# Performance work log

Measured on AMD Instinct MI355X. Metric: run time of the kernel, lower is better.

The kernel has to match this reference:

```python
import jax, jax.numpy as jnp
import numpy as np

SEQ = 110          # input_size1 = sample_width*2
HALF = SEQ // 2    # 55
N_EMBD = 102       # n_chrom + 2
HEAD = 192

def _cross_half_mask():
    # attention allowed only between the two halves (same-half blocks masked)
    idx = jnp.arange(SEQ)
    same_half = (idx[:, None] < HALF) == (idx[None, :] < HALF)
    return same_half  # True where attention is DISALLOWED

def setup_inputs() -> dict:
    key = jax.random.key(0)
    k1, k2, k3, k4 = jax.random.split(key, 4)
    B = 8192
    x = jax.random.normal(k1, (B, SEQ, N_EMBD), dtype=jnp.float32)
    Wq = jax.random.normal(k2, (N_EMBD, HEAD), dtype=jnp.float32) * (N_EMBD ** -0.5)
    Wk = jax.random.normal(k3, (N_EMBD, HEAD), dtype=jnp.float32) * (N_EMBD ** -0.5)
    Wv = jax.random.normal(k4, (N_EMBD, HEAD), dtype=jnp.float32) * (N_EMBD ** -0.5)
    return {"x": x, "Wq": Wq, "Wk": Wk, "Wv": Wv}

def reference(x, Wq, Wk, Wv):
    # q,k,v: [B, S, H]
    q = x @ Wq
    k = x @ Wk
    v = x @ Wv
    scale = HEAD ** -0.5
    scores = jnp.einsum('bsh,bth->bst', q, k) * scale  # [B, S, S]
    mask = _cross_half_mask()                           # [S, S] True = masked
    scores = jnp.where(mask, -jnp.inf, scores)
    attn = jax.nn.softmax(scores, axis=-1)
    # dropout is identity at inference (p=0.15 at train)
    out = jnp.einsum('bst,bth->bsh', attn, v)           # [B, S, H]
    return out
```

## Files before the change

### kernel.cpp

```cpp
#include <hip/hip_runtime.h>
#include <hip/hip_bf16.h>

#define SEQ   110
#define HALFS 55
#define EMB   102
#define HEAD  192

typedef short bf16x8 __attribute__((ext_vector_type(8)));
typedef float f32x4  __attribute__((ext_vector_type(4)));

#define XS    104
#define XTILE (64 * XS)
#define PS    72
#define MTS   128
#define MTROWS 112
#define MT_SHORTS (MTROWS * MTS)
#define WES   128

__device__ __forceinline__ short f2bf(float f) {
    unsigned u = __float_as_uint(f);
    unsigned r = u + 0x7fffu + ((u >> 16) & 1u);
    return (short)(r >> 16);
}
__device__ __forceinline__ unsigned pk2(float a, float b) {
    return ((unsigned)(unsigned short)f2bf(b) << 16) | (unsigned short)f2bf(a);
}

__global__ void prep(const float* __restrict__ Wq, const float* __restrict__ Wk,
                     const float* __restrict__ Wv, short* __restrict__ ws) {
    int flat = blockIdx.x * 256 + threadIdx.x;
    if (flat < MT_SHORTS) {
        int i = flat >> 7, j = flat & 127;
        float v = 0.0f;
        if (i < EMB && j < EMB) {
            const float4* q4 = (const float4*)(Wq + j * HEAD);
            const float4* k4 = (const float4*)(Wk + i * HEAD);
            float s = 0.0f;
            #pragma unroll 4
            for (int h4 = 0; h4 < HEAD / 4; ++h4) {
                float4 a = q4[h4], b = k4[h4];
                s += a.x * b.x + a.y * b.y + a.z * b.z + a.w * b.w;
            }
            v = s * 0.07216878364870322f;
        }
        ws[flat] = f2bf(v);
    } else if (flat < MT_SHORTS + HEAD * WES) {
        int idx = flat - MT_SHORTS;
        int h = idx >> 7, e = idx & 127;
        float v = (e < EMB) ? Wv[e * HEAD + h] : 0.0f;
        ws[flat] = f2bf(v);
    }
}

__global__ __launch_bounds__(512, 2)
void attn_head(const float* __restrict__ x, const short* __restrict__ ws,
               float* __restrict__ out, int B) {
    const int tid  = threadIdx.x;
    const int w8   = tid >> 6;
    const int h    = w8 >> 2;
    const int w4   = w8 & 3;
    const int lane = tid & 63;
    const int g    = lane >> 4;
    const int r    = lane & 15;

    __shared__ __attribute__((aligned(16))) short u[4 * XTILE];
    __shared__ __attribute__((aligned(16))) short P_lds[2][64 * PS];

    short* xh = u + h * XTILE;
    short* xo = u + (h ^ 1) * XTILE;
    short* yh = u + (2 + h) * XTILE;
    short* Ph = P_lds[h];

    const short* Mt  = ws;
    const short* WvT = ws + MT_SHORTS;

    bf16x8 wvf[3][4];
    #pragma unroll
    for (int mi = 0; mi < 3; ++mi) {
        const int hrow = 16 * (w4 + 4 * mi) + r;
        #pragma unroll
        for (int kk = 0; kk < 4; ++kk)
            wvf[mi][kk] = *(const bf16x8*)(WvT + hrow * WES + 32 * kk + 8 * g);
    }

    {
        unsigned long long* z = (unsigned long long*)u;
        if (tid < 468) z[(tid < 234 ? 1430 : 2860) + tid] = 0ull;
        if (tid < 110)
            *(unsigned*)(u + (tid & 1) * XTILE + (tid >> 1) * XS + 102) = 0u;
    }

    unsigned xv0[6], xv1[6];
    auto loadx = [&](int batch) {
        const float4* xb4 = (const float4*)(x + (size_t)batch * (SEQ * EMB));
        #pragma unroll
        for (int it = 0; it < 6; ++it) {
            int i4 = tid + it * 512;
            if (i4 < 2805) { float4 v = xb4[i4]; xv0[it] = pk2(v.x, v.y); xv1[it] = pk2(v.z, v.w); }
        }
    };
    auto stagex = [&]() {
        #pragma unroll
        for (int it = 0; it < 6; ++it) {
            int i4 = tid + it * 512;
            if (i4 < 2805) {
                int fc  = i4 * 4;
                int row = (int)(((unsigned long long)fc * 41121ull) >> 22);
                int e   = fc - row * EMB;
                int tile = row >= HALFS;
                int lr   = row - HALFS * tile;
                int ba   = tile * XTILE + lr * XS + e;
                if (e == 100) {
                    int rowb  = row + 1;
                    int tileb = rowb >= HALFS;
                    int lrb   = rowb - HALFS * tileb;
                    *(unsigned*)(u + ba) = xv0[it];
                    *(unsigned*)(u + tileb * XTILE + lrb * XS) = xv1[it];
                } else {
                    uint2 t2; t2.x = xv0[it]; t2.y = xv1[it];
                    *(uint2*)(u + ba) = t2;
                }
            }
        }
    };

    loadx(blockIdx.x);
    const int stride = (int)gridDim.x;

    bf16x8 ax[4][4];
    bf16x8 zz = {};

    #pragma unroll 1
    for (int p = blockIdx.x; p < B; p += stride) {
        stagex();
        __syncthreads();

        bf16x8 am[2][4];
        #pragma unroll
        for (int mi2 = 0; mi2 < 2; ++mi2) {
            const int mt = w4 + 4 * mi2;
            #pragma unroll
            for (int kk = 0; kk < 4; ++kk)
                am[mi2][kk] = (mt < 7) ? *(const bf16x8*)(Mt + (16 * mt + r) * MTS + 32 * kk + 8 * g) : zz;
        }

        #pragma unroll
        for (int stl = 0; stl < 4; ++stl) {
            const short* xb = xh + (16 * stl + r) * XS;
            bf16x8 bx[4];
            #pragma unroll
            for (int kk = 0; kk < 3; ++kk) bx[kk] = *(const bf16x8*)(xb + 32 * kk + 8 * g);
            bx[3] = zz;
            if (g == 0) bx[3] = *(const bf16x8*)(xb + 96);
            #pragma unroll
            for (int mi2 = 0; mi2 < 2; ++mi2) {
                const int mt = w4 + 4 * mi2;
                if (mt < 7) {
                    f32x4 acc = {0.f, 0.f, 0.f, 0.f};
                    #pragma unroll
                    for (int kk = 0; kk < 4; ++kk)
                        acc = __builtin_amdgcn_mfma_f32_16x16x32_bf16(am[mi2][kk], bx[kk], acc, 0, 0, 0);
                    if (mt < 6 || g < 2) {
                        uint2 t2; t2.x = pk2(acc[0], acc[1]); t2.y = pk2(acc[2], acc[3]);
                        *(uint2*)(yh + (16 * stl + r) * XS + 16 * mt + 4 * g) = t2;
                    }
                }
            }
        }

        #pragma unroll
        for (int mt = 0; mt < 4; ++mt) {
            const short* xb = xo + (16 * mt + r) * XS;
            #pragma unroll
            for (int kk = 0; kk < 3; ++kk) ax[mt][kk] = *(const bf16x8*)(xb + 32 * kk + 8 * g);
            ax[mt][3] = zz;
            if (g == 0) ax[mt][3] = *(const bf16x8*)(xb + 96);
        }

        unsigned vpk[4][3][2];
        #pragma unroll
        for (int st = 0; st < 4; ++st) {
            #pragma unroll
            for (int mi = 0; mi < 3; ++mi) {
                f32x4 acc = {0.f, 0.f, 0.f, 0.f};
                #pragma unroll
                for (int kk = 0; kk < 4; ++kk)
                    acc = __builtin_amdgcn_mfma_f32_16x16x32_bf16(ax[st][kk], wvf[mi][kk], acc, 0, 0, 0);
                vpk[st][mi][0] = pk2(acc[0], acc[1]);
                vpk[st][mi][1] = pk2(acc[2], acc[3]);
            }
        }
        const int src0 = ((g & 1) << 5) + r;
        const int src1 = src0 + 16;
        const bool hi  = (g >> 1) != 0;
        bf16x8 va[3][2];
        #pragma unroll
        for (int mi = 0; mi < 3; ++mi) {
            unsigned e00 = (unsigned)__shfl((int)vpk[0][mi][0], src0), e01 = (unsigned)__shfl((int)vpk[0][mi][1], src0);
            unsigned e02 = (unsigned)__shfl((int)vpk[0][mi][0], src1), e03 = (unsigned)__shfl((int)vpk[0][mi][1], src1);
            unsigned f00 = (unsigned)__shfl((int)vpk[1][mi][0], src0), f01 = (unsigned)__shfl((int)vpk[1][mi][1], src0);
            unsigned f02 = (unsigned)__shfl((int)vpk[1][mi][0], src1), f03 = (unsigned)__shfl((int)vpk[1][mi][1], src1);
            uint4 u0;
            u0.x = hi ? f00 : e00; u0.y = hi ? f01 : e01; u0.z = hi ? f02 : e02; u0.w = hi ? f03 : e03;
            unsigned e10 = (unsigned)__shfl((int)vpk[2][mi][0], src0), e11 = (unsigned)__shfl((int)vpk[2][mi][1], src0);
            unsigned e12 = (unsigned)__shfl((int)vpk[2][mi][0], src1), e13 = (unsigned)__shfl((int)vpk[2][mi][1], src1);
            unsigned f10 = (unsigned)__shfl((int)vpk[3][mi][0], src0), f11 = (unsigned)__shfl((int)vpk[3][mi][1], src0);
            unsigned f12 = (unsigned)__shfl((int)vpk[3][mi][0], src1), f13 = (unsigned)__shfl((int)vpk[3][mi][1], src1);
            uint4 u1;
            u1.x = hi ? f10 : e10; u1.y = hi ? f11 : e11; u1.z = hi ? f12 : e12; u1.w = hi ? f13 : e13;
            __builtin_memcpy(&va[mi][0], &u0, 16);
            __builtin_memcpy(&va[mi][1], &u1, 16);
        }

        __syncthreads();

        if (p + stride < B) loadx(p + stride);

        {
            const short* yb = yh + (16 * w4 + r) * XS;
            bf16x8 by[4];
            #pragma unroll
            for (int kk = 0; kk < 3; ++kk) by[kk] = *(const bf16x8*)(yb + 32 * kk + 8 * g);
            by[3] = zz;
            if (g == 0) by[3] = *(const bf16x8*)(yb + 96);

            float sc[4][4];
            #pragma unroll
            for (int mt = 0; mt < 4; ++mt) {
                f32x4 acc = {0.f, 0.f, 0.f, 0.f};
                #pragma unroll
                for (int kk = 0; kk < 4; ++kk)
                    acc = __builtin_amdgcn_mfma_f32_16x16x32_bf16(ax[mt][kk], by[kk], acc, 0, 0, 0);
                #pragma unroll
                for (int j = 0; j < 4; ++j) sc[mt][j] = acc[j];
            }
            #pragma unroll
            for (int j = 0; j < 4; ++j)
                if (48 + 4 * g + j >= HALFS) sc[3][j] = -1e30f;

            float mx = -1e30f;
            #pragma unroll
            for (int mt = 0; mt < 4; ++mt) {
                #pragma unroll
                for (int j = 0; j < 4; ++j) mx = fmaxf(mx, sc[mt][j]);
            }
            mx = fmaxf(mx, __shfl_xor(mx, 16));
            mx = fmaxf(mx, __shfl_xor(mx, 32));
            float pr[4][4];
            float sum = 0.f;
            #pragma unroll
            for (int mt = 0; mt < 4; ++mt) {
                #pragma unroll
                for (int j = 0; j < 4; ++j) { pr[mt][j] = __expf(sc[mt][j] - mx); sum += pr[mt][j]; }
            }
            sum += __shfl_xor(sum, 16);
            sum += __shfl_xor(sum, 32);
            float rs = 1.0f / sum;

            #pragma unroll
            for (int mt = 0; mt < 4; ++mt) {
                uint2 t2;
                t2.x = pk2(pr[mt][0] * rs, pr[mt][1] * rs);
                t2.y = pk2(pr[mt][2] * rs, pr[mt][3] * rs);
                *(uint2*)(Ph + (16 * w4 + r) * PS + 16 * mt + 4 * g) = t2;
            }
        }
        __syncthreads();

        const size_t obase = (size_t)p * (SEQ * HEAD) + (size_t)(h * HALFS) * HEAD;
        #pragma unroll
        for (int c = 0; c < 4; ++c) {
            const short* pb = Ph + (16 * c + r) * PS + 8 * g;
            bf16x8 bp0 = *(const bf16x8*)(pb);
            bf16x8 bp1 = *(const bf16x8*)(pb + 32);
            const int srow  = 16 * c + r;
            const bool valid = srow < HALFS;
            float* orow = out + obase + (size_t)srow * HEAD;
            #pragma unroll
            for (int mi = 0; mi < 3; ++mi) {
                f32x4 acc = {0.f, 0.f, 0.f, 0.f};
                acc = __builtin_amdgcn_mfma_f32_16x16x32_bf16(va[mi][0], bp0, acc, 0, 0, 0);
                acc = __builtin_amdgcn_mfma_f32_16x16x32_bf16(va[mi][1], bp1, acc, 0, 0, 0);
                if (valid) {
                    float4 st4; st4.x = acc[0]; st4.y = acc[1]; st4.z = acc[2]; st4.w = acc[3];
                    *(float4*)(orow + 16 * (w4 + 4 * mi) + 4 * g) = st4;
                }
            }
        }
        __syncthreads();
    }
}

extern "C" void kernel_launch(void* const* d_in, const int* in_sizes, int n_in,
                              void* d_out, int out_size, void* d_ws, size_t ws_size,
                              hipStream_t stream) {
    const float* x  = (const float*)d_in[0];
    const float* Wq = (const float*)d_in[1];
    const float* Wk = (const float*)d_in[2];
    const float* Wv = (const float*)d_in[3];
    short* ws = (short*)d_ws;
    int B = in_sizes[0] / (SEQ * EMB);
    int prep_elems = MT_SHORTS + HEAD * WES;
    prep<<<(prep_elems + 255) / 256, 256, 0, stream>>>(Wq, Wk, Wv, ws);
    attn_head<<<512, 512, 0, stream>>>(x, ws, (float*)d_out, B);
}
```

Measured before the change: 303.1 us.

## Keep projected Y in registers, restructure loop to cut LDS and barriers

Each wave now computes its own 16-row slice of the x·M projection directly, using Mt fragments loaded in the inner loop. The result is redistributed through lane shuffles into B-operand fragments instead of being written to an LDS Y tile and read back. This removes half of the x LDS buffer and two of the four barriers per iteration. The global prefetch of the next sample is issued at the start of the iteration and staged into LDS after the barrier, overlapping with the P·V output phase. The cost is more global/L2 reads of Mt per iteration, higher register pressure, and a tighter correctness dependency on barrier placement for the staged x buffer.

```diff
diff --git a/kernel.cpp b/kernel.cpp
--- a/kernel.cpp
+++ b/kernel.cpp
@@ -63,12 +63,11 @@
     const int g    = lane >> 4;
     const int r    = lane & 15;
 
-    __shared__ __attribute__((aligned(16))) short u[4 * XTILE];
+    __shared__ __attribute__((aligned(16))) short u[2 * XTILE];
     __shared__ __attribute__((aligned(16))) short P_lds[2][64 * PS];
 
     short* xh = u + h * XTILE;
     short* xo = u + (h ^ 1) * XTILE;
-    short* yh = u + (2 + h) * XTILE;
     short* Ph = P_lds[h];
 
     const short* Mt  = ws;
@@ -125,47 +124,58 @@
     };
 
     loadx(blockIdx.x);
+    stagex();
     const int stride = (int)gridDim.x;
 
     bf16x8 ax[4][4];
     bf16x8 zz = {};
+    const int src0 = ((g & 1) << 5) + r;
+    const int src1 = src0 + 16;
+    const bool hi  = (g >> 1) != 0;
 
     #pragma unroll 1
     for (int p = blockIdx.x; p < B; p += stride) {
-        stagex();
         __syncthreads();
 
-        bf16x8 am[2][4];
-        #pragma unroll
-        for (int mi2 = 0; mi2 < 2; ++mi2) {
-            const int mt = w4 + 4 * mi2;
-            #pragma unroll
-            for (int kk = 0; kk < 4; ++kk)
-                am[mi2][kk] = (mt < 7) ? *(const bf16x8*)(Mt + (16 * mt + r) * MTS + 32 * kk + 8 * g) : zz;
-        }
-
-        #pragma unroll
-        for (int stl = 0; stl < 4; ++stl) {
-            const short* xb = xh + (16 * stl + r) * XS;
-            bf16x8 bx[4];
+        if (p + stride < B) loadx(p + stride);
+
+        bf16x8 bx[4];
+        {
+            const short* xb = xh + (16 * w4 + r) * XS;
             #pragma unroll
             for (int kk = 0; kk < 3; ++kk) bx[kk] = *(const bf16x8*)(xb + 32 * kk + 8 * g);
             bx[3] = zz;
             if (g == 0) bx[3] = *(const bf16x8*)(xb + 96);
-            #pragma unroll
-            for (int mi2 = 0; mi2 < 2; ++mi2) {
-                const int mt = w4 + 4 * mi2;
-                if (mt < 7) {
-                    f32x4 acc = {0.f, 0.f, 0.f, 0.f};
-                    #pragma unroll
-                    for (int kk = 0; kk < 4; ++kk)
-                        acc = __builtin_amdgcn_mfma_f32_16x16x32_bf16(am[mi2][kk], bx[kk], acc, 0, 0, 0);
-                    if (mt < 6 || g < 2) {
-                        uint2 t2; t2.x = pk2(acc[0], acc[1]); t2.y = pk2(acc[2], acc[3]);
-                        *(uint2*)(yh + (16 * stl + r) * XS + 16 * mt + 4 * g) = t2;
-                    }
-                }
-            }
+        }
+
+        unsigned vyp[8][2];
+        #pragma unroll
+        for (int mt = 0; mt < 7; ++mt) {
+            f32x4 acc = {0.f, 0.f, 0.f, 0.f};
+            #pragma unroll
+            for (int kk = 0; kk < 4; ++kk) {
+                bf16x8 am = *(const bf16x8*)(Mt + (16 * mt + r) * MTS + 32 * kk + 8 * g);
+                acc = __builtin_amdgcn_mfma_f32_16x16x32_bf16(am, bx[kk], acc, 0, 0, 0);
+            }
+            vyp[mt][0] = pk2(acc[0], acc[1]);
+            vyp[mt][1] = pk2(acc[2], acc[3]);
+        }
+        vyp[7][0] = 0u; vyp[7][1] = 0u;
+
+        bf16x8 by[4];
+        #pragma unroll
+        for (int kk = 0; kk < 4; ++kk) {
+            unsigned e0 = (unsigned)__shfl((int)vyp[2 * kk][0],     src0);
+            unsigned e1 = (unsigned)__shfl((int)vyp[2 * kk][1],     src0);
+            unsigned e2 = (unsigned)__shfl((int)vyp[2 * kk][0],     src1);
+            unsigned e3 = (unsigned)__shfl((int)vyp[2 * kk][1],     src1);
+            unsigned f0 = (unsigned)__shfl((int)vyp[2 * kk + 1][0], src0);
+            unsigned f1 = (unsigned)__shfl((int)vyp[2 * kk + 1][1], src0);
+            unsigned f2 = (unsigned)__shfl((int)vyp[2 * kk + 1][0], src1);
+            unsigned f3 = (unsigned)__shfl((int)vyp[2 * kk + 1][1], src1);
+            uint4 q;
+            q.x = hi ? f0 : e0; q.y = hi ? f1 : e1; q.z = hi ? f2 : e2; q.w = hi ? f3 : e3;
+            __builtin_memcpy(&by[kk], &q, 16);
         }
 
         #pragma unroll
@@ -175,6 +185,49 @@
             for (int kk = 0; kk < 3; ++kk) ax[mt][kk] = *(const bf16x8*)(xb + 32 * kk + 8 * g);
             ax[mt][3] = zz;
             if (g == 0) ax[mt][3] = *(const bf16x8*)(xb + 96);
+        }
+
+        {
+            float sc[4][4];
+            #pragma unroll
+            for (int mt = 0; mt < 4; ++mt) {
+                f32x4 acc = {0.f, 0.f, 0.f, 0.f};
+                #pragma unroll
+                for (int kk = 0; kk < 4; ++kk)
+                    acc = __builtin_amdgcn_mfma_f32_16x16x32_bf16(ax[mt][kk], by[kk], acc, 0, 0, 0);
+                #pragma unroll
+                for (int j = 0; j < 4; ++j) sc[mt][j] = acc[j];
+            }
+            #pragma unroll
+            for (int j = 0; j < 4; ++j)
+                if (48 + 4 * g + j >= HALFS) sc[3][j] = -1e30f;
+
+            float mx = -1e30f;
+            #pragma unroll
+            for (int mt = 0; mt < 4; ++mt) {
+                #pragma unroll
+                for (int j = 0; j < 4; ++j) mx = fmaxf(mx, sc[mt][j]);
+            }
+            mx = fmaxf(mx, __shfl_xor(mx, 16));
+            mx = fmaxf(mx, __shfl_xor(mx, 32));
+            float pr[4][4];
+            float sum = 0.f;
+            #pragma unroll
+            for (int mt = 0; mt < 4; ++mt) {
+                #pragma unroll
+                for (int j = 0; j < 4; ++j) { pr[mt][j] = __expf(sc[mt][j] - mx); sum += pr[mt][j]; }
+            }
+            sum += __shfl_xor(sum, 16);
+            sum += __shfl_xor(sum, 32);
+            float rs = 1.0f / sum;
+
+            #pragma unroll
+            for (int mt = 0; mt < 4; ++mt) {
+                uint2 t2;
+                t2.x = pk2(pr[mt][0] * rs, pr[mt][1] * rs);
+                t2.y = pk2(pr[mt][2] * rs, pr[mt][3] * rs);
+                *(uint2*)(Ph + (16 * w4 + r) * PS + 16 * mt + 4 * g) = t2;
+            }
         }
 
         unsigned vpk[4][3][2];
@@ -190,9 +243,6 @@
                 vpk[st][mi][1] = pk2(acc[2], acc[3]);
             }
         }
-        const int src0 = ((g & 1) << 5) + r;
-        const int src1 = src0 + 16;
-        const bool hi  = (g >> 1) != 0;
         bf16x8 va[3][2];
         #pragma unroll
         for (int mi = 0; mi < 3; ++mi) {
@@ -214,58 +264,7 @@
 
         __syncthreads();
 
-        if (p + stride < B) loadx(p + stride);
-
-        {
-            const short* yb = yh + (16 * w4 + r) * XS;
-            bf16x8 by[4];
-            #pragma unroll
-            for (int kk = 0; kk < 3; ++kk) by[kk] = *(const bf16x8*)(yb + 32 * kk + 8 * g);
-            by[3] = zz;
-            if (g == 0) by[3] = *(const bf16x8*)(yb + 96);
-
-            float sc[4][4];
-            #pragma unroll
-            for (int mt = 0; mt < 4; ++mt) {
-                f32x4 acc = {0.f, 0.f, 0.f, 0.f};
-                #pragma unroll
-                for (int kk = 0; kk < 4; ++kk)
-                    acc = __builtin_amdgcn_mfma_f32_16x16x32_bf16(ax[mt][kk], by[kk], acc, 0, 0, 0);
-                #pragma unroll
-                for (int j = 0; j < 4; ++j) sc[mt][j] = acc[j];
-            }
-            #pragma unroll
-            for (int j = 0; j < 4; ++j)
-                if (48 + 4 * g + j >= HALFS) sc[3][j] = -1e30f;
-
-            float mx = -1e30f;
-            #pragma unroll
-            for (int mt = 0; mt < 4; ++mt) {
-                #pragma unroll
-                for (int j = 0; j < 4; ++j) mx = fmaxf(mx, sc[mt][j]);
-            }
-            mx = fmaxf(mx, __shfl_xor(mx, 16));
-            mx = fmaxf(mx, __shfl_xor(mx, 32));
-            float pr[4][4];
-            float sum = 0.f;
-            #pragma unroll
-            for (int mt = 0; mt < 4; ++mt) {
-                #pragma unroll
-                for (int j = 0; j < 4; ++j) { pr[mt][j] = __expf(sc[mt][j] - mx); sum += pr[mt][j]; }
-            }
-            sum += __shfl_xor(sum, 16);
-            sum += __shfl_xor(sum, 32);
-            float rs = 1.0f / sum;
-
-            #pragma unroll
-            for (int mt = 0; mt < 4; ++mt) {
-                uint2 t2;
-                t2.x = pk2(pr[mt][0] * rs, pr[mt][1] * rs);
-                t2.y = pk2(pr[mt][2] * rs, pr[mt][3] * rs);
-                *(uint2*)(Ph + (16 * w4 + r) * PS + 16 * mt + 4 * g) = t2;
-            }
-        }
-        __syncthreads();
+        if (p + stride < B) stagex();
 
         const size_t obase = (size_t)p * (SEQ * HEAD) + (size_t)(h * HALFS) * HEAD;
         #pragma unroll
@@ -287,7 +286,6 @@
                 }
             }
         }
-        __syncthreads();
     }
 }
 
```

Result: slower. 521.7 us (+72.1%).
